# Kernel optimization log

Hardware: AMD Instinct MI355X
Metric: run time of the kernel (lower is better)

The kernel has to match this reference:

```python
import jax, jax.numpy as jnp
import numpy as np

SPATIAL_SHAPES = [(128, 128), (64, 64), (32, 32), (16, 16)]  # H,W per level
B, H, D = 4, 8, 32          # batch, heads, head_dim
Q, L, P = 10000, 4, 4       # queries, levels, points
S = sum(h * w for h, w in SPATIAL_SHAPES)  # 21760


def setup_inputs() -> dict:
    key = jax.random.key(0)
    k1, k2, k3 = jax.random.split(key, 3)
    value = jax.random.normal(k1, (B, S, H, D), dtype=jnp.float32)
    sampling_locations = jax.random.uniform(k2, (B, Q, H, L, P, 2), dtype=jnp.float32)
    aw = jax.random.uniform(k3, (B, Q, H, L, P), dtype=jnp.float32)
    # normalize like the real module does (softmax over levels*points)
    attention_weights = aw / aw.sum(axis=(3, 4), keepdims=True)
    spatial = jnp.asarray(SPATIAL_SHAPES, dtype=jnp.int32)
    lsi = jnp.asarray(np.cumsum([0] + [h * w for h, w in SPATIAL_SHAPES[:-1]]), dtype=jnp.int32)
    return {
        "value": value,
        "value_spatial_shapes": spatial,
        "level_start_index": lsi,
        "sampling_locations": sampling_locations,
        "attention_weights": attention_weights,
        "im2col_step": 64,
    }


def _sample_level(vflat, x, y, h, w):
    """Bilinear sample with zero padding, align_corners=False.
    vflat: [B,H,h*w,D]; x,y: [B,H,Q,P] pixel coords. Returns [B,H,Q,P,D]."""
    x0f = jnp.floor(x)
    y0f = jnp.floor(y)
    fx = x - x0f
    fy = y - y0f
    x0 = x0f.astype(jnp.int32)
    y0 = y0f.astype(jnp.int32)

    def corner(iy, ix, wgt):
        valid = (iy >= 0) & (iy < h) & (ix >= 0) & (ix < w)
        idx = jnp.clip(iy, 0, h - 1) * w + jnp.clip(ix, 0, w - 1)  # [B,H,Q,P]
        b, nh, q, p = idx.shape
        v = jnp.take_along_axis(vflat, idx.reshape(b, nh, q * p, 1), axis=2)
        v = v.reshape(b, nh, q, p, -1)
        return v * (wgt * valid)[..., None]

    return (corner(y0, x0, (1 - fx) * (1 - fy))
            + corner(y0, x0 + 1, fx * (1 - fy))
            + corner(y0 + 1, x0, (1 - fx) * fy)
            + corner(y0 + 1, x0 + 1, fx * fy))


def _ms_deform_attn(value, sampling_locations, attention_weights, shapes_list):
    b, _, nh, d = value.shape
    q = sampling_locations.shape[1]
    grids = 2.0 * sampling_locations - 1.0  # [B,Q,H,L,P,2] in [-1,1]
    offsets = np.cumsum([0] + [h * w for h, w in shapes_list])
    out = jnp.zeros((b, nh, q, d), dtype=value.dtype)
    for lvl, (h, w) in enumerate(shapes_list):
        # value for this level: [B,H,h*w,D]
        v = jax.lax.slice_in_dim(value, int(offsets[lvl]), int(offsets[lvl + 1]), axis=1)
        vflat = v.transpose(0, 2, 1, 3)
        g = grids[:, :, :, lvl].transpose(0, 2, 1, 3, 4)  # [B,H,Q,P,2]
        # grid_sample align_corners=False pixel coords
        x = (g[..., 0] + 1.0) * (w * 0.5) - 0.5
        y = (g[..., 1] + 1.0) * (h * 0.5) - 0.5
        sampled = _sample_level(vflat, x, y, h, w)  # [B,H,Q,P,D]
        aw = attention_weights[:, :, :, lvl].transpose(0, 2, 1, 3)  # [B,H,Q,P]
        out = out + jnp.sum(sampled * aw[..., None], axis=3)
    # [B,H,Q,D] -> [B,Q,H*D]
    return out.transpose(0, 2, 1, 3).reshape(b, q, nh * d)


def reference(value, value_spatial_shapes, level_start_index, sampling_locations, attention_weights, im2col_step):
    # spatial shapes are static metadata (define tensor shapes), so read concretely
    shapes_list = [tuple(int(v) for v in row) for row in np.asarray(value_spatial_shapes)]
    return _ms_deform_attn(value, sampling_locations, attention_weights, shapes_list)
```

## Files before the change

### kernel.cpp

```cpp
#include <hip/hip_runtime.h>
#include <hip/hip_fp16.h>


#define MSDA_B 4
#define MSDA_Q 10000
#define MSDA_H 8
#define MSDA_D 32
#define MSDA_L 4
#define MSDA_P 4
#define MSDA_S 21760

#define MSDA_QBLK16 157
#define MSDA_QBLK32 313

#define MSDA_NB 16
#define MSDA_QPC 640
#define MSDA_LDS_BYTES 81920

__global__ __launch_bounds__(256) void msda_convert_kernel(
    const float* __restrict__ value, __half* __restrict__ vw)
{
    int o4 = blockIdx.x * 256 + threadIdx.x;
    int d4 = o4 & 7;
    int rest = o4 >> 3;
    int s = rest % MSDA_S;
    int bh = rest / MSDA_S;
    int b = bh >> 3, h = bh & 7;
    float4 v = *(const float4*)(value +
        (((size_t)b * MSDA_S + s) * MSDA_H + h) * MSDA_D + 4 * d4);
    union { __half2 h2[2]; uint2 u; } pk;
    pk.h2[0] = __floats2half2_rn(v.x, v.y);
    pk.h2[1] = __floats2half2_rn(v.z, v.w);
    ((uint2*)vw)[o4] = pk.u;
}

__global__ __launch_bounds__(512, 2) void msda_fwd_lds_kernel(
    const __half* __restrict__ vw,
    const float* __restrict__ loc,
    const float* __restrict__ aw,
    float* __restrict__ out)
{
    constexpr int H = MSDA_H, D = MSDA_D, L = MSDA_L, P = MSDA_P;
    constexpr int Q = MSDA_Q, S = MSDA_S;
    const int lvl_sh[4]    = {7, 6, 5, 4};
    const int lvl_start[4] = {0, 16384, 20480, 21504};
    const int lvl_lstart[4] = {0, 0, 0, 1024};

    extern __shared__ char smem[];

    int i = blockIdx.x;
    int h = i & 7;
    int r = i >> 3;
    int qc = r & (MSDA_NB - 1);
    int b = r >> 4;

    const size_t slice = (size_t)(b * H + h) * S * D;

    {
        const uint4* src = (const uint4*)(vw + slice + (size_t)20480 * D);
        uint4* dst = (uint4*)smem;
#pragma unroll
        for (int k = 0; k < 10; ++k)
            dst[threadIdx.x + 512 * k] = src[threadIdx.x + 512 * k];
    }
    __syncthreads();

    const int lane = threadIdx.x & 3;
    const unsigned coff = (unsigned)lane * 16;
    const int qsub = threadIdx.x >> 2;
    const char* vb = (const char*)(vw + slice);

    for (int it = 0; it < MSDA_QPC / 128; ++it) {
        int q = qc * MSDA_QPC + it * 128 + qsub;
        if (q >= Q) break;

        const size_t bqh = ((size_t)b * Q + q) * H + h;
        const float4* lp4 = (const float4*)(loc + bqh * (L * P * 2));
        const float4* wp4 = (const float4*)(aw  + bqh * (L * P));

        float2 acc[4] = {{0.f,0.f},{0.f,0.f},{0.f,0.f},{0.f,0.f}};

#pragma unroll
        for (int l = 0; l < L; ++l) {
            const int sh = lvl_sh[l];
            const int hw = 1 << sh;
            const float fhw = (float)hw;

            float4 la = lp4[2 * l + 0];
            float4 lb = lp4[2 * l + 1];
            float4 wv = wp4[l];
            float lx[4] = {la.x, la.z, lb.x, lb.z};
            float ly[4] = {la.y, la.w, lb.y, lb.w};
            float wl[4] = {wv.x, wv.y, wv.z, wv.w};

#pragma unroll
            for (int p = 0; p < P; ++p) {
                float x = lx[p] * fhw - 0.5f;
                float y = ly[p] * fhw - 0.5f;
                float xf = floorf(x), yf = floorf(y);
                float fx = x - xf, fy = y - yf;
                int x0 = (int)xf, y0 = (int)yf;
                int x1 = x0 + 1, y1 = y0 + 1;

                float vx0 = ((unsigned)x0 < (unsigned)hw) ? 1.f : 0.f;
                float vx1 = ((unsigned)x1 < (unsigned)hw) ? 1.f : 0.f;
                float vy0 = ((unsigned)y0 < (unsigned)hw) ? 1.f : 0.f;
                float vy1 = ((unsigned)y1 < (unsigned)hw) ? 1.f : 0.f;

                int cx0 = min(max(x0, 0), hw - 1);
                int cx1 = min(max(x1, 0), hw - 1);
                int cy0 = min(max(y0, 0), hw - 1);
                int cy1 = min(max(y1, 0), hw - 1);

                int r0 = cy0 << sh;
                int r1 = cy1 << sh;

                union U { uint4 u; __half2 h2[4]; };
                U u00, u01, u10, u11;

                if (l < 2) {
                    const int start = lvl_start[l];
                    unsigned o00 = ((unsigned)(start + r0 + cx0) << 6) + coff;
                    unsigned o01 = ((unsigned)(start + r0 + cx1) << 6) + coff;
                    unsigned o10 = ((unsigned)(start + r1 + cx0) << 6) + coff;
                    unsigned o11 = ((unsigned)(start + r1 + cx1) << 6) + coff;
                    u00.u = *(const uint4*)(vb + o00);
                    u01.u = *(const uint4*)(vb + o01);
                    u10.u = *(const uint4*)(vb + o10);
                    u11.u = *(const uint4*)(vb + o11);
                } else {
                    const int lstart = lvl_lstart[l];
                    unsigned o00 = ((unsigned)(lstart + r0 + cx0) << 6) + coff;
                    unsigned o01 = ((unsigned)(lstart + r0 + cx1) << 6) + coff;
                    unsigned o10 = ((unsigned)(lstart + r1 + cx0) << 6) + coff;
                    unsigned o11 = ((unsigned)(lstart + r1 + cx1) << 6) + coff;
                    u00.u = *(const uint4*)(smem + o00);
                    u01.u = *(const uint4*)(smem + o01);
                    u10.u = *(const uint4*)(smem + o10);
                    u11.u = *(const uint4*)(smem + o11);
                }

                float wgt = wl[p];
                float w00 = (1.f - fx) * (1.f - fy) * wgt * vx0 * vy0;
                float w01 = fx * (1.f - fy) * wgt * vx1 * vy0;
                float w10 = (1.f - fx) * fy * wgt * vx0 * vy1;
                float w11 = fx * fy * wgt * vx1 * vy1;

#pragma unroll
                for (int j = 0; j < 4; ++j) {
                    float2 f00 = __half22float2(u00.h2[j]);
                    float2 f01 = __half22float2(u01.h2[j]);
                    float2 f10 = __half22float2(u10.h2[j]);
                    float2 f11 = __half22float2(u11.h2[j]);
                    acc[j].x += w00 * f00.x + w01 * f01.x + w10 * f10.x + w11 * f11.x;
                    acc[j].y += w00 * f00.y + w01 * f01.y + w10 * f10.y + w11 * f11.y;
                }
            }
        }

        float4* op = (float4*)out + bqh * (D / 4) + lane * 2;
        op[0] = make_float4(acc[0].x, acc[0].y, acc[1].x, acc[1].y);
        op[1] = make_float4(acc[2].x, acc[2].y, acc[3].x, acc[3].y);
    }
}

__global__ __launch_bounds__(256) void msda_fwd_fp16_kernel(
    const __half* __restrict__ vw, const float* __restrict__ loc,
    const float* __restrict__ aw, float* __restrict__ out)
{
    constexpr int H = MSDA_H, D = MSDA_D, L = MSDA_L, P = MSDA_P;
    constexpr int S = MSDA_S, Q = MSDA_Q;
    const int lvl_sh[4]    = {7, 6, 5, 4};
    const int lvl_start[4] = {0, 16384, 20480, 21504};

    int i = blockIdx.x;
    int h = i & 7;
    int r = i >> 3;
    int b = r / MSDA_QBLK16;
    int qb = r - b * MSDA_QBLK16;

    int q = qb * 64 + (threadIdx.x >> 2);
    if (q >= Q) return;
    const int lane = threadIdx.x & 3;
    const unsigned coff = (unsigned)lane * 16;

    const size_t bqh = ((size_t)b * Q + q) * H + h;
    const float4* lp4 = (const float4*)(loc + bqh * (L * P * 2));
    const float4* wp4 = (const float4*)(aw  + bqh * (L * P));
    const char* vb = (const char*)(vw + (size_t)(b * H + h) * S * D);

    float2 acc[4] = {{0.f,0.f},{0.f,0.f},{0.f,0.f},{0.f,0.f}};

#pragma unroll
    for (int l = 0; l < L; ++l) {
        const int sh = lvl_sh[l];
        const int hw = 1 << sh;
        const float fhw = (float)hw;
        const int start = lvl_start[l];

        float4 la = lp4[2 * l + 0];
        float4 lb = lp4[2 * l + 1];
        float4 wv = wp4[l];
        float lx[4] = {la.x, la.z, lb.x, lb.z};
        float ly[4] = {la.y, la.w, lb.y, lb.w};
        float wl[4] = {wv.x, wv.y, wv.z, wv.w};

#pragma unroll
        for (int p = 0; p < P; ++p) {
            float x = lx[p] * fhw - 0.5f;
            float y = ly[p] * fhw - 0.5f;
            float xf = floorf(x), yf = floorf(y);
            float fx = x - xf, fy = y - yf;
            int x0 = (int)xf, y0 = (int)yf;
            int x1 = x0 + 1, y1 = y0 + 1;

            float vx0 = ((unsigned)x0 < (unsigned)hw) ? 1.f : 0.f;
            float vx1 = ((unsigned)x1 < (unsigned)hw) ? 1.f : 0.f;
            float vy0 = ((unsigned)y0 < (unsigned)hw) ? 1.f : 0.f;
            float vy1 = ((unsigned)y1 < (unsigned)hw) ? 1.f : 0.f;

            int cx0 = min(max(x0, 0), hw - 1);
            int cx1 = min(max(x1, 0), hw - 1);
            int cy0 = min(max(y0, 0), hw - 1);
            int cy1 = min(max(y1, 0), hw - 1);

            int r0 = start + (cy0 << sh);
            int r1 = start + (cy1 << sh);
            unsigned o00 = ((unsigned)(r0 + cx0) << 6) + coff;
            unsigned o01 = ((unsigned)(r0 + cx1) << 6) + coff;
            unsigned o10 = ((unsigned)(r1 + cx0) << 6) + coff;
            unsigned o11 = ((unsigned)(r1 + cx1) << 6) + coff;

            union U { uint4 u; __half2 h2[4]; };
            U u00, u01, u10, u11;
            u00.u = *(const uint4*)(vb + o00);
            u01.u = *(const uint4*)(vb + o01);
            u10.u = *(const uint4*)(vb + o10);
            u11.u = *(const uint4*)(vb + o11);

            float wgt = wl[p];
            float w00 = (1.f - fx) * (1.f - fy) * wgt * vx0 * vy0;
            float w01 = fx * (1.f - fy) * wgt * vx1 * vy0;
            float w10 = (1.f - fx) * fy * wgt * vx0 * vy1;
            float w11 = fx * fy * wgt * vx1 * vy1;

#pragma unroll
            for (int j = 0; j < 4; ++j) {
                float2 f00 = __half22float2(u00.h2[j]);
                float2 f01 = __half22float2(u01.h2[j]);
                float2 f10 = __half22float2(u10.h2[j]);
                float2 f11 = __half22float2(u11.h2[j]);
                acc[j].x += w00 * f00.x + w01 * f01.x + w10 * f10.x + w11 * f11.x;
                acc[j].y += w00 * f00.y + w01 * f01.y + w10 * f10.y + w11 * f11.y;
            }
        }
    }

    float4* op = (float4*)out + bqh * (D / 4) + lane * 2;
    op[0] = make_float4(acc[0].x, acc[0].y, acc[1].x, acc[1].y);
    op[1] = make_float4(acc[2].x, acc[2].y, acc[3].x, acc[3].y);
}

__global__ __launch_bounds__(256, 4) void msda_fwd_fp32_kernel(
    const float* __restrict__ value, const float* __restrict__ loc,
    const float* __restrict__ aw, float* __restrict__ out)
{
    constexpr int H = MSDA_H, D = MSDA_D, L = MSDA_L, P = MSDA_P;
    constexpr int S = MSDA_S, Q = MSDA_Q;
    const int lvl_sh[4]    = {7, 6, 5, 4};
    const int lvl_start[4] = {0, 16384, 20480, 21504};

    int i = blockIdx.x;
    int h = i & 7;
    int r = i >> 3;
    int b = r / MSDA_QBLK32;
    int qb = r - b * MSDA_QBLK32;

    int q = qb * 32 + (threadIdx.x >> 3);
    if (q >= Q) return;
    const unsigned coff = (threadIdx.x & 7) * 16;

    const size_t bqh = ((size_t)b * Q + q) * H + h;
    const float4* lp4 = (const float4*)(loc + bqh * (L * P * 2));
    const float4* wp4 = (const float4*)(aw  + bqh * (L * P));
    const char* vb = (const char*)(value + ((size_t)b * S * H + h) * D);

    float4 acc = {0.f, 0.f, 0.f, 0.f};

#pragma unroll
    for (int l = 0; l < L; ++l) {
        const int sh = lvl_sh[l];
        const int hw = 1 << sh;
        const float fhw = (float)hw;
        const int start = lvl_start[l];

        float4 la = lp4[2 * l + 0];
        float4 lb = lp4[2 * l + 1];
        float4 wv = wp4[l];
        float lx[4] = {la.x, la.z, lb.x, lb.z};
        float ly[4] = {la.y, la.w, lb.y, lb.w};
        float wl[4] = {wv.x, wv.y, wv.z, wv.w};

#pragma unroll
        for (int p = 0; p < P; ++p) {
            float x = lx[p] * fhw - 0.5f;
            float y = ly[p] * fhw - 0.5f;
            float xf = floorf(x), yf = floorf(y);
            float fx = x - xf, fy = y - yf;
            int x0 = (int)xf, y0 = (int)yf;
            int x1 = x0 + 1, y1 = y0 + 1;

            float vx0 = ((unsigned)x0 < (unsigned)hw) ? 1.f : 0.f;
            float vx1 = ((unsigned)x1 < (unsigned)hw) ? 1.f : 0.f;
            float vy0 = ((unsigned)y0 < (unsigned)hw) ? 1.f : 0.f;
            float vy1 = ((unsigned)y1 < (unsigned)hw) ? 1.f : 0.f;

            int cx0 = min(max(x0, 0), hw - 1);
            int cx1 = min(max(x1, 0), hw - 1);
            int cy0 = min(max(y0, 0), hw - 1);
            int cy1 = min(max(y1, 0), hw - 1);

            float wgt = wl[p];
            float w00 = (1.f - fx) * (1.f - fy) * wgt * vx0 * vy0;
            float w01 = fx * (1.f - fy) * wgt * vx1 * vy0;
            float w10 = (1.f - fx) * fy * wgt * vx0 * vy1;
            float w11 = fx * fy * wgt * vx1 * vy1;

            int r0 = start + (cy0 << sh);
            int r1 = start + (cy1 << sh);
            unsigned o00 = ((unsigned)(r0 + cx0) << 10) + coff;
            unsigned o01 = ((unsigned)(r0 + cx1) << 10) + coff;
            unsigned o10 = ((unsigned)(r1 + cx0) << 10) + coff;
            unsigned o11 = ((unsigned)(r1 + cx1) << 10) + coff;

            float4 v00 = *(const float4*)(vb + o00);
            float4 v01 = *(const float4*)(vb + o01);
            float4 v10 = *(const float4*)(vb + o10);
            float4 v11 = *(const float4*)(vb + o11);

            acc.x += w00 * v00.x + w01 * v01.x + w10 * v10.x + w11 * v11.x;
            acc.y += w00 * v00.y + w01 * v01.y + w10 * v10.y + w11 * v11.y;
            acc.z += w00 * v00.z + w01 * v01.z + w10 * v10.z + w11 * v11.z;
            acc.w += w00 * v00.w + w01 * v01.w + w10 * v10.w + w11 * v11.w;
        }
    }

    ((float4*)out)[bqh * (D / 4) + (threadIdx.x & 7)] = acc;
}

extern "C" void kernel_launch(void* const* d_in, const int* in_sizes, int n_in,
                              void* d_out, int out_size, void* d_ws, size_t ws_size,
                              hipStream_t stream) {
    const float* value = (const float*)d_in[0];
    const float* loc = (const float*)d_in[3];
    const float* aw  = (const float*)d_in[4];
    float* out = (float*)d_out;

    static int lds_ok = -1;
    if (lds_ok < 0) {
        hipError_t e = hipFuncSetAttribute(
            reinterpret_cast<const void*>(msda_fwd_lds_kernel),
            hipFuncAttributeMaxDynamicSharedMemorySize, MSDA_LDS_BYTES);
        lds_ok = (e == hipSuccess) ? 1 : 0;
    }

    const size_t need = (size_t)MSDA_B * MSDA_H * MSDA_S * MSDA_D * sizeof(__half);
    if (ws_size >= need) {
        __half* vw = (__half*)d_ws;
        msda_convert_kernel<<<(MSDA_B * MSDA_S * MSDA_H * MSDA_D / 4 + 255) / 256,
                              256, 0, stream>>>(value, vw);
        if (lds_ok) {
            const int grid = MSDA_B * MSDA_H * MSDA_NB;
            msda_fwd_lds_kernel<<<grid, 512, MSDA_LDS_BYTES, stream>>>(vw, loc, aw, out);
        } else {
            const int grid = 8 * MSDA_B * MSDA_QBLK16;
            msda_fwd_fp16_kernel<<<grid, 256, 0, stream>>>(vw, loc, aw, out);
        }
    } else {
        const int grid = 8 * MSDA_B * MSDA_QBLK32;
        msda_fwd_fp32_kernel<<<grid, 256, 0, stream>>>(value, loc, aw, out);
    }
}
```

Measured before the change: 275.9 us.

## Accumulate bilinear samples in packed half2 FMA and halve query-chunk grid

```diff
diff --git a/kernel.cpp b/kernel.cpp
--- a/kernel.cpp
+++ b/kernel.cpp
@@ -13,8 +13,8 @@
 #define MSDA_QBLK16 157
 #define MSDA_QBLK32 313
 
-#define MSDA_NB 16
-#define MSDA_QPC 640
+#define MSDA_NB 8
+#define MSDA_QPC 1250
 #define MSDA_LDS_BYTES 81920
 
 __global__ __launch_bounds__(256) void msda_convert_kernel(
@@ -42,8 +42,8 @@
 {
     constexpr int H = MSDA_H, D = MSDA_D, L = MSDA_L, P = MSDA_P;
     constexpr int Q = MSDA_Q, S = MSDA_S;
-    const int lvl_sh[4]    = {7, 6, 5, 4};
-    const int lvl_start[4] = {0, 16384, 20480, 21504};
+    const int lvl_sh[4]     = {7, 6, 5, 4};
+    const int lvl_start[4]  = {0, 16384, 20480, 21504};
     const int lvl_lstart[4] = {0, 0, 0, 1024};
 
     extern __shared__ char smem[];
@@ -52,7 +52,7 @@
     int h = i & 7;
     int r = i >> 3;
     int qc = r & (MSDA_NB - 1);
-    int b = r >> 4;
+    int b = r >> 3;
 
     const size_t slice = (size_t)(b * H + h) * S * D;
 
@@ -70,9 +70,12 @@
     const int qsub = threadIdx.x >> 2;
     const char* vb = (const char*)(vw + slice);
 
-    for (int it = 0; it < MSDA_QPC / 128; ++it) {
-        int q = qc * MSDA_QPC + it * 128 + qsub;
-        if (q >= Q) break;
+    const int qcbase = qc * MSDA_QPC;
+
+    for (int it = 0; it < 10; ++it) {
+        int off = it * 128 + qsub;
+        if (off >= MSDA_QPC) break;
+        int q = qcbase + off;
 
         const size_t bqh = ((size_t)b * Q + q) * H + h;
         const float4* lp4 = (const float4*)(loc + bqh * (L * P * 2));
@@ -92,6 +95,12 @@
             float lx[4] = {la.x, la.z, lb.x, lb.z};
             float ly[4] = {la.y, la.w, lb.y, lb.w};
             float wl[4] = {wv.x, wv.y, wv.z, wv.w};
+
+            __half2 acch[4];
+            acch[0] = __float2half2_rn(0.f);
+            acch[1] = __float2half2_rn(0.f);
+            acch[2] = __float2half2_rn(0.f);
+            acch[3] = __float2half2_rn(0.f);
 
 #pragma unroll
             for (int p = 0; p < P; ++p) {
@@ -146,15 +155,25 @@
                 float w10 = (1.f - fx) * fy * wgt * vx0 * vy1;
                 float w11 = fx * fy * wgt * vx1 * vy1;
 
+                __half2 W00 = __float2half2_rn(w00);
+                __half2 W01 = __float2half2_rn(w01);
+                __half2 W10 = __float2half2_rn(w10);
+                __half2 W11 = __float2half2_rn(w11);
+
 #pragma unroll
                 for (int j = 0; j < 4; ++j) {
-                    float2 f00 = __half22float2(u00.h2[j]);
-                    float2 f01 = __half22float2(u01.h2[j]);
-                    float2 f10 = __half22float2(u10.h2[j]);
-                    float2 f11 = __half22float2(u11.h2[j]);
-                    acc[j].x += w00 * f00.x + w01 * f01.x + w10 * f10.x + w11 * f11.x;
-                    acc[j].y += w00 * f00.y + w01 * f01.y + w10 * f10.y + w11 * f11.y;
+                    acch[j] = __hfma2(u00.h2[j], W00, acch[j]);
+                    acch[j] = __hfma2(u01.h2[j], W01, acch[j]);
+                    acch[j] = __hfma2(u10.h2[j], W10, acch[j]);
+                    acch[j] = __hfma2(u11.h2[j], W11, acch[j]);
                 }
+            }
+
+#pragma unroll
+            for (int j = 0; j < 4; ++j) {
+                float2 t = __half22float2(acch[j]);
+                acc[j].x += t.x;
+                acc[j].y += t.y;
             }
         }
 
```

Measured after the change: 267.3 us. 1.03x faster.
